# Optimization experiments

Hardware: AMD Instinct MI355X
Metric: run time of the kernel (lower is better)

Reference implementation:

```python
import jax, jax.numpy as jnp
import numpy as np

N = 100000   # nodes
E = 1600000  # edges
G = 64       # graphs in batch
D = 128      # node_dim
H = 128      # hid_dim
OUT = 10     # out_dim (classes)
L = 3        # max_layer GIN layers per branch
BN_EPS = 1e-5


def setup_inputs() -> dict:
    key = jax.random.key(0)
    ks = jax.random.split(key, 24)
    p = lambda k, shape: (jax.random.normal(k, shape, jnp.float32) * 0.05)
    inp = {
        "x": jax.random.normal(ks[0], (N, D), jnp.float32),
        "edge_index": jax.random.randint(ks[1], (2, E), 0, N, jnp.int32),
        "batch": jnp.sort(jax.random.randint(ks[2], (N,), 0, G, jnp.int32)),
        # branch A: conv1 + convs  (stacked per-layer params; node_dim == hid_dim)
        "W1a": p(ks[3], (L, D, H)), "b1a": p(ks[4], (L, H)),
        "W2a": p(ks[5], (L, H, H)), "b2a": p(ks[6], (L, H)),
        "ga": jnp.ones((L, H), jnp.float32), "bta": jnp.zeros((L, H), jnp.float32),
        # branch B: conv2 + convs2
        "W1b": p(ks[7], (L, D, H)), "b1b": p(ks[8], (L, H)),
        "W2b": p(ks[9], (L, H, H)), "b2b": p(ks[10], (L, H)),
        "gb": jnp.ones((L, H), jnp.float32), "btb": jnp.zeros((L, H), jnp.float32),
        # heads
        "lin1_w": p(ks[11], (2 * H, H)), "lin1_b": p(ks[12], (H,)),
        "lin2_w": p(ks[13], (H, OUT)), "lin2_b": p(ks[14], (OUT,)),
        # bilinear discriminator (nn.Bilinear(H, H, 1))
        "disc_w": p(ks[15], (H, H)), "disc_b": jnp.zeros((), jnp.float32),
    }
    return inp


def _gin(h, src, dst, W1, b1, W2, b2, g, bt):
    # GINConv (eps=0): MLP(x + sum_{j->i} x_j); MLP = Lin-ReLU-Lin-ReLU-BN
    agg = jax.ops.segment_sum(h[src], dst, num_segments=N)  # scatter-add over edges
    h = h + agg
    h = jax.nn.relu(h @ W1 + b1)
    h = jax.nn.relu(h @ W2 + b2)
    mu = h.mean(0)
    var = jnp.mean((h - mu) ** 2, axis=0)
    return (h - mu) * jax.lax.rsqrt(var + BN_EPS) * g + bt


def reference(x, edge_index, batch, W1a, b1a, W2a, b2a, ga, bta,
              W1b, b1b, W2b, b2b, gb, btb, lin1_w, lin1_b, lin2_w, lin2_b,
              disc_w, disc_b):
    src, dst = edge_index[0], edge_index[1]
    counts = jnp.clip(jax.ops.segment_sum(jnp.ones((N,), x.dtype), batch, num_segments=G), 1.0)

    # branch A: conv1 + convs -> per-graph mean pool
    h = x
    for i in range(L):
        h = _gin(h, src, dst, W1a[i], b1a[i], W2a[i], b2a[i], ga[i], bta[i])
    mean_a = jax.ops.segment_sum(h, batch, num_segments=G) / counts[:, None]  # [G,H]

    # branch B (subgraph branch, run on the same graph): conv2 + convs2 -> pool
    hb = x
    for i in range(L):
        hb = _gin(hb, src, dst, W1b[i], b1b[i], W2b[i], b2b[i], gb[i], btb[i])
    pool_x = jax.ops.segment_sum(hb, batch, num_segments=G) / counts[:, None]  # [G,H]

    # MI discriminator: shuffle index as in Net.MI
    idx = jnp.arange(G - 1, -1, -1)
    idx = idx.at[G // 2].set(idx[G // 2 + 1])
    shuffled = pool_x[idx]
    bil = lambda a, c: jnp.einsum('gd,de,ge->g', a, disc_w, c) + disc_b
    logits = jnp.concatenate([bil(pool_x, pool_x), bil(pool_x, shuffled)])  # [2G]

    # classification head: cat(mean_pool, pool_x) -> lin1 -> relu -> lin2 -> log_softmax
    z = jnp.concatenate([mean_a, pool_x], axis=-1)
    z = jax.nn.relu(z @ lin1_w + lin1_b)
    z = z @ lin2_w + lin2_b
    predicts = jax.nn.log_softmax(z, axis=-1)  # [G,OUT]

    return jnp.concatenate([predicts.ravel(), logits.ravel()])  # [G*OUT + 2G]
```

## Files before the change

### kernel.cpp

```cpp
#include <hip/hip_runtime.h>
#include <hip/hip_bf16.h>

#define NN 100000
#define EE 1600000
#define GG 64
#define HH 128
#define LL 3
#define BN_EPS 1e-5f
#define NBUCK 196
#define BCAP 12288
#define PART_CHUNK 8192
#define NREP 16

typedef __attribute__((ext_vector_type(8))) short bf16x8;
typedef __attribute__((ext_vector_type(4))) float f32x4;
typedef unsigned int uint32;

__device__ __forceinline__ unsigned short f2bf(float f) {
    uint32 x = __float_as_uint(f);
    uint32 r = (x + 0x7fffu + ((x >> 16) & 1u)) >> 16;
    return (unsigned short)r;
}
__device__ __forceinline__ float bf2f(unsigned short u) { return __uint_as_float(((uint32)u) << 16); }
__device__ __forceinline__ void accq(float4& a, uint32 u, float sc) {
    a.x += sc * (float)(u & 0xffu);
    a.y += sc * (float)((u >> 8) & 0xffu);
    a.z += sc * (float)((u >> 16) & 0xffu);
    a.w += sc * (float)(u >> 24);
}
__device__ __forceinline__ uint32 ld32(const unsigned char* p, uint32 off) {
    return *(const uint32*)(p + off);
}
__device__ __forceinline__ float ldf(const float* p, uint32 byteoff) {
    return *(const float*)((const char*)p + byteoff);
}

__global__ __launch_bounds__(256) void partition_kernel(
    const int* __restrict__ src, const int* __restrict__ dst,
    int* __restrict__ bcnt, uint32* __restrict__ part) {
    __shared__ int cnt[NBUCK];
    __shared__ int loff[NBUCK + 1];
    __shared__ int gpos[NBUCK];
    __shared__ int lcur[NBUCK];
    __shared__ uint32 buf[PART_CHUNK];
    int tid = threadIdx.x;
    int base = blockIdx.x * PART_CHUNK;
    int n = min(PART_CHUNK, EE - base);
    for (int i = tid; i < NBUCK; i += 256) { cnt[i] = 0; lcur[i] = 0; }
    __syncthreads();
    for (int i = tid; i < n; i += 256) atomicAdd(&cnt[dst[base + i] >> 9], 1);
    __syncthreads();
    if (tid == 0) {
        int acc = 0;
        for (int b = 0; b < NBUCK; ++b) { loff[b] = acc; acc += cnt[b]; }
        loff[NBUCK] = acc;
    }
    __syncthreads();
    if (tid < NBUCK && cnt[tid] > 0) gpos[tid] = atomicAdd(&bcnt[tid], cnt[tid]);
    __syncthreads();
    for (int i = tid; i < n; i += 256) {
        int d = dst[base + i];
        int s = src[base + i];
        int b = d >> 9;
        int slot = atomicAdd(&lcur[b], 1);
        buf[loff[b] + slot] = (uint32)s | ((uint32)(d & 511) << 17);
    }
    __syncthreads();
    for (int i = tid; i < n; i += 256) {
        int lo = 0, hi = NBUCK;
        while (hi - lo > 1) { int mid = (lo + hi) >> 1; if (loff[mid] <= i) lo = mid; else hi = mid; }
        part[(size_t)lo * BCAP + gpos[lo] + (i - loff[lo])] = buf[i];
    }
}

__global__ __launch_bounds__(256) void build_col_kernel(
    const uint32* __restrict__ part, const int* __restrict__ bcnt,
    int* __restrict__ col, int2* __restrict__ rowpair) {
    __shared__ int ldeg[512];
    __shared__ int loffn[512];
    __shared__ int lcur[512];
    __shared__ int pscan[256];
    __shared__ int cl[BCAP];
    int b = blockIdx.x;
    int tid = threadIdx.x;
    int node0 = b << 9;
    int nn = min(node0 + 512, NN) - node0;
    int cnt = bcnt[b];
    int base = b * BCAP;
    const uint32* pp = part + (size_t)base;
    for (int i = tid; i < 512; i += 256) { ldeg[i] = 0; lcur[i] = 0; }
    __syncthreads();
    for (int i = tid; i < cnt; i += 256) atomicAdd(&ldeg[pp[i] >> 17], 1);
    __syncthreads();
    int t2 = tid * 2;
    int a0 = ldeg[t2], a1 = ldeg[t2 + 1];
    int ps = a0 + a1;
    pscan[tid] = ps;
    __syncthreads();
    for (int off = 1; off < 256; off <<= 1) {
        int v = (tid >= off) ? pscan[tid - off] : 0;
        __syncthreads();
        pscan[tid] += v;
        __syncthreads();
    }
    int eo = pscan[tid] - ps;
    loffn[t2] = eo;
    loffn[t2 + 1] = eo + a0;
    if (t2 < nn)     rowpair[node0 + t2]     = make_int2(base + eo, base + eo + a0);
    if (t2 + 1 < nn) rowpair[node0 + t2 + 1] = make_int2(base + eo + a0, base + eo + a0 + a1);
    __syncthreads();
    for (int i = tid; i < cnt; i += 256) {
        uint32 v = pp[i];
        int dl = (int)(v >> 17);
        int pos = atomicAdd(&lcur[dl], 1);
        cl[loffn[dl] + pos] = (int)(v & 0x1FFFFu);
    }
    __syncthreads();
    for (int i = tid; i < cnt; i += 256) col[base + i] = cl[i];
}

__global__ void counts_kernel(const int* __restrict__ batch, float* __restrict__ cnt, int n) {
    __shared__ int h[GG];
    int tid = threadIdx.x;
    if (tid < GG) h[tid] = 0;
    __syncthreads();
    int i = blockIdx.x * 256 + tid;
    if (i < n) atomicAdd(&h[batch[i]], 1);
    __syncthreads();
    if (tid < GG && h[tid]) atomicAdd(&cnt[tid], (float)h[tid]);
}

__global__ void x_to_i8_kernel(const float* __restrict__ x, unsigned short* __restrict__ x8,
                               float* __restrict__ sc0) {
    int row = (blockIdx.x * 256 + threadIdx.x) >> 6;
    int lane = threadIdx.x & 63;
    if (row >= NN) return;
    float2 v = ((const float2*)x)[(size_t)row * 64 + lane];
    float m = fmaxf(fabsf(v.x), fabsf(v.y));
#pragma unroll
    for (int off = 1; off < 64; off <<= 1) m = fmaxf(m, __shfl_xor(m, off));
    float scale = m * (1.f / 127.f);
    float inv = (m > 0.f) ? 127.f / m : 0.f;
    int b0 = __float2int_rn(v.x * inv) + 128;
    int b1 = __float2int_rn(v.y * inv) + 128;
    unsigned short pk = (unsigned short)((b0 & 0xff) | ((b1 & 0xff) << 8));
    x8[(size_t)row * 64 + lane] = pk;
    if (lane == 0) sc0[row] = scale;
}

#define MAT_STRIDE 16384

__global__ void convert_w_kernel(const float* __restrict__ W1a, const float* __restrict__ W2a,
                                 const float* __restrict__ W1b, const float* __restrict__ W2b,
                                 unsigned short* __restrict__ out) {
    int t = blockIdx.x * 256 + threadIdx.x;
    if (t >= 24576) return;
    int lane = t & 63;
    int r = t >> 6;
    int ks = r & 3; r >>= 2;
    int nt = r & 7; r >>= 3;
    int mat = r & 1; r >>= 1;
    int l = r % 3, br = r / 3;
    const float* W = br ? (mat ? W2b : W1b) : (mat ? W2a : W1a);
    const float* Wl = W + (size_t)l * 128 * 128;
    int n0 = nt * 16 + (lane & 15);
    int k0 = ks * 32 + (lane >> 4) * 8;
    unsigned short tmp[8];
#pragma unroll
    for (int j = 0; j < 8; ++j) tmp[j] = f2bf(Wl[(size_t)(k0 + j) * 128 + n0]);
    size_t seq = (size_t)(br * 3 + l) * 2 + mat;
    size_t off = (((seq * 8 + nt) * 4 + ks) * 64 + (size_t)lane) * 8;
    *(uint4*)(out + off) = *(const uint4*)tmp;
}

__global__ void bn_coefs_kernel(const float* __restrict__ statsRep,
                                const float* __restrict__ ga, const float* __restrict__ bta,
                                const float* __restrict__ gb, const float* __restrict__ btb,
                                int l, float* __restrict__ coef) {
    int t = threadIdx.x;
    int br = t >> 7, cc = t & 127;
    const float* base = statsRep + (size_t)((l * 2 + br) * NREP) * 256;
    float s = 0.f, sq = 0.f;
#pragma unroll
    for (int rep = 0; rep < NREP; ++rep) {
        s += base[rep * 256 + cc];
        sq += base[rep * 256 + 128 + cc];
    }
    float mu = s * (1.f / NN);
    float var = sq * (1.f / NN) - mu * mu;
    float gm = (br ? gb : ga)[l * 128 + cc];
    float A = gm * rsqrtf(var + BN_EPS);
    float B = (br ? btb : bta)[l * 128 + cc] - mu * A;
    coef[br * 256 + cc] = A;
    coef[br * 256 + 128 + cc] = B;
}

__global__ __launch_bounds__(256) void gather0_kernel(
    const unsigned char* __restrict__ x8b, const float* __restrict__ sc0,
    const int2* __restrict__ rowpair, const int* __restrict__ col,
    uint2* __restrict__ out) {
    int gw = (blockIdx.x * blockDim.x + threadIdx.x) >> 6;
    int lane = threadIdx.x & 63;
    if (gw >= NN) return;
    int slot = lane >> 5;
    int c = lane & 31;
    uint32 c4 = (uint32)c << 2;
    float4 accA = {0.f, 0.f, 0.f, 0.f};
    float4 accB = {0.f, 0.f, 0.f, 0.f};
    float S = 0.f;
    if (slot == 0) {
        float s = sc0[gw];
        uint32 u = ld32(x8b, ((uint32)gw << 7) + c4);
        accq(accA, u, s);
        S += s;
    }
    int2 be = rowpair[gw];
    int beg = be.x, end = be.y;
    for (int base = beg; base < end; base += 64) {
        int nb = min(64, end - base);
        int colv = col[base + min(lane, nb - 1)];
        int k = 0;
        for (; k + 4 <= nb; k += 4) {
            int j0 = __shfl(colv, k + slot);
            int j1 = __shfl(colv, k + 2 + slot);
            float s0 = ldf(sc0, (uint32)j0 << 2);
            float s1 = ldf(sc0, (uint32)j1 << 2);
            uint32 u0 = ld32(x8b, ((uint32)j0 << 7) + c4);
            uint32 u1 = ld32(x8b, ((uint32)j1 << 7) + c4);
            accq(accA, u0, s0); S += s0;
            accq(accB, u1, s1); S += s1;
        }
        for (; k + 2 <= nb; k += 2) {
            int j = __shfl(colv, k + slot);
            float s = ldf(sc0, (uint32)j << 2);
            uint32 u = ld32(x8b, ((uint32)j << 7) + c4);
            accq(accA, u, s); S += s;
        }
        if (k < nb) {
            int j = __shfl(colv, k);
            if (slot == 0) {
                float s = ldf(sc0, (uint32)j << 2);
                uint32 u = ld32(x8b, ((uint32)j << 7) + c4);
                accq(accA, u, s); S += s;
            }
        }
    }
    accA.x += accB.x; accA.y += accB.y; accA.z += accB.z; accA.w += accB.w;
    accA.x += __shfl_xor(accA.x, 32);
    accA.y += __shfl_xor(accA.y, 32);
    accA.z += __shfl_xor(accA.z, 32);
    accA.w += __shfl_xor(accA.w, 32);
    S += __shfl_xor(S, 32);
    float f0 = accA.x - 128.f * S;
    float f1 = accA.y - 128.f * S;
    float f2 = accA.z - 128.f * S;
    float f3 = accA.w - 128.f * S;
    if (slot == 0) {
        uint2 o;
        o.x = (uint32)f2bf(f0) | ((uint32)f2bf(f1) << 16);
        o.y = (uint32)f2bf(f2) | ((uint32)f2bf(f3) << 16);
        out[(uint32)gw * 32 + c] = o;
    }
}

__global__ __launch_bounds__(256) void gather_dual_kernel(
    const unsigned char* __restrict__ y8, const float* __restrict__ scales,
    const int2* __restrict__ rowpair, const int* __restrict__ col,
    const float* __restrict__ coef, uint2* __restrict__ out) {
    int gw = (blockIdx.x * blockDim.x + threadIdx.x) >> 6;
    int lane = threadIdx.x & 63;
    if (gw >= NN) return;
    int br = lane >> 5;
    int c32 = lane & 31;
    uint32 ln4 = (uint32)lane << 2;
    uint32 sb4 = (uint32)br << 2;
    float4 A4 = ((const float4*)(coef + br * 256))[c32];
    float4 B4 = ((const float4*)(coef + br * 256 + 128))[c32];
    float4 accA = {0.f, 0.f, 0.f, 0.f};
    float4 accB = {0.f, 0.f, 0.f, 0.f};
    {
        float s = ldf(scales, ((uint32)gw << 3) + sb4);
        uint32 u = ld32(y8, ((uint32)gw << 8) + ln4);
        accq(accA, u, s);
    }
    int2 be = rowpair[gw];
    int beg = be.x, end = be.y;
    float degp1 = (float)(end - beg + 1);
    for (int base = beg; base < end; base += 64) {
        int nb = min(64, end - base);
        int colv = col[base + min(lane, nb - 1)];
        int k = 0;
        for (; k + 4 <= nb; k += 4) {
            int j0 = __builtin_amdgcn_readlane(colv, k);
            int j1 = __builtin_amdgcn_readlane(colv, k + 1);
            int j2 = __builtin_amdgcn_readlane(colv, k + 2);
            int j3 = __builtin_amdgcn_readlane(colv, k + 3);
            float s0 = ldf(scales, ((uint32)j0 << 3) + sb4);
            float s1 = ldf(scales, ((uint32)j1 << 3) + sb4);
            float s2 = ldf(scales, ((uint32)j2 << 3) + sb4);
            float s3 = ldf(scales, ((uint32)j3 << 3) + sb4);
            uint32 u0 = ld32(y8, ((uint32)j0 << 8) + ln4);
            uint32 u1 = ld32(y8, ((uint32)j1 << 8) + ln4);
            uint32 u2 = ld32(y8, ((uint32)j2 << 8) + ln4);
            uint32 u3 = ld32(y8, ((uint32)j3 << 8) + ln4);
            accq(accA, u0, s0);
            accq(accB, u1, s1);
            accq(accA, u2, s2);
            accq(accB, u3, s3);
        }
        for (; k < nb; ++k) {
            int j = __builtin_amdgcn_readlane(colv, k);
            float s = ldf(scales, ((uint32)j << 3) + sb4);
            uint32 u = ld32(y8, ((uint32)j << 8) + ln4);
            accq(accA, u, s);
        }
    }
    float o0 = A4.x * (accA.x + accB.x) + B4.x * degp1;
    float o1 = A4.y * (accA.y + accB.y) + B4.y * degp1;
    float o2 = A4.z * (accA.z + accB.z) + B4.z * degp1;
    float o3 = A4.w * (accA.w + accB.w) + B4.w * degp1;
    uint2 o;
    o.x = (uint32)f2bf(o0) | ((uint32)f2bf(o1) << 16);
    o.y = (uint32)f2bf(o2) | ((uint32)f2bf(o3) << 16);
    out[(size_t)gw * 64 + lane] = o;
}

#define LDS_W1 16384
#define LDS_HS (8 * 16 * 136)
__global__ __launch_bounds__(512, 4) void mlp_dual_kernel(
    const unsigned short* __restrict__ X, int in_stride, int in_off_mul,
    const unsigned short* __restrict__ wf_all,
    const float* __restrict__ b1a, const float* __restrict__ b1b,
    const float* __restrict__ b2a, const float* __restrict__ b2b,
    int l, int quant,
    unsigned short* __restrict__ Y, unsigned char* __restrict__ Y8,
    float* __restrict__ scales, float* __restrict__ statsRep, int n) {
    extern __shared__ unsigned short lds_all[];
    unsigned short* w1s = lds_all;
    unsigned short (*hs)[16][136] = (unsigned short (*)[16][136])(lds_all + LDS_W1);
    float* ssum = (float*)(lds_all + LDS_W1 + LDS_HS);
    float* ssq = ssum + 128;

    int br = blockIdx.y;
    const unsigned short* Wf = wf_all + (size_t)(br * 3 + l) * 2 * MAT_STRIDE;
    const float* b1 = (br ? b1b : b1a) + l * 128;
    const float* b2 = (br ? b2b : b2a) + l * 128;
    float* statsp = statsRep + (size_t)((l * 2 + br) * NREP + (blockIdx.x & (NREP - 1))) * 256;
    int in_off = in_off_mul * br;

    int tid = threadIdx.x;
    int wv = tid >> 6, lane = tid & 63;
    int quad = lane >> 4, l16 = lane & 15;

    const bf16x8* w2g = (const bf16x8*)(Wf + MAT_STRIDE);

    bf16x8 w2p[2][4];
#pragma unroll
    for (int p = 0; p < 2; ++p)
#pragma unroll
        for (int ks = 0; ks < 4; ++ks) w2p[p][ks] = w2g[(p * 4 + ks) * 64 + lane];

    int row0 = blockIdx.x * 128 + wv * 16;

    bf16x8 aF[4];
    {
        int r = row0 + l16;
        if (r >= n) r = n - 1;
        const unsigned short* xrow = X + (size_t)r * in_stride + in_off;
#pragma unroll
        for (int ks = 0; ks < 4; ++ks) aF[ks] = *(const bf16x8*)(xrow + ks * 32 + quad * 8);
    }

    {
        const uint4* srcp = (const uint4*)Wf;
        uint4* dstp = (uint4*)w1s;
        for (int i = tid; i < 2048; i += 512) dstp[i] = srcp[i];
    }
    if (tid < 128) { ssum[tid] = 0.f; ssq[tid] = 0.f; }
    __syncthreads();

    f32x4 acc1[8];
#pragma unroll
    for (int nt = 0; nt < 8; ++nt) {
        f32x4 c = {0.f, 0.f, 0.f, 0.f};
#pragma unroll
        for (int ks = 0; ks < 4; ++ks) {
            bf16x8 bfrag = *(const bf16x8*)(&w1s[((nt * 4 + ks) * 64 + lane) * 8]);
            c = __builtin_amdgcn_mfma_f32_16x16x32_bf16(aF[ks], bfrag, c, 0, 0, 0);
        }
        acc1[nt] = c;
    }

#pragma unroll
    for (int nt = 0; nt < 8; ++nt) {
        int c0 = nt * 16 + l16;
        float bb = b1[c0];
#pragma unroll
        for (int r = 0; r < 4; ++r) {
            float v = fmaxf(acc1[nt][r] + bb, 0.f);
            hs[wv][quad * 4 + r][c0] = f2bf(v);
        }
    }

    bf16x8 aH[4];
#pragma unroll
    for (int ks = 0; ks < 4; ++ks)
        aH[ks] = *(const bf16x8*)(&hs[wv][l16][ks * 32 + quad * 8]);

    f32x4 acc2_[8];
#pragma unroll
    for (int nt = 0; nt < 8; ++nt) {
        bf16x8 bf0, bf1, bf2, bf3;
        if (nt < 2) { bf0 = w2p[nt][0]; bf1 = w2p[nt][1]; bf2 = w2p[nt][2]; bf3 = w2p[nt][3]; }
        else {
            bf0 = w2g[(nt * 4 + 0) * 64 + lane];
            bf1 = w2g[(nt * 4 + 1) * 64 + lane];
            bf2 = w2g[(nt * 4 + 2) * 64 + lane];
            bf3 = w2g[(nt * 4 + 3) * 64 + lane];
        }
        f32x4 c = {0.f, 0.f, 0.f, 0.f};
        c = __builtin_amdgcn_mfma_f32_16x16x32_bf16(aH[0], bf0, c, 0, 0, 0);
        c = __builtin_amdgcn_mfma_f32_16x16x32_bf16(aH[1], bf1, c, 0, 0, 0);
        c = __builtin_amdgcn_mfma_f32_16x16x32_bf16(aH[2], bf2, c, 0, 0, 0);
        c = __builtin_amdgcn_mfma_f32_16x16x32_bf16(aH[3], bf3, c, 0, 0, 0);
        acc2_[nt] = c;
    }

#pragma unroll
    for (int nt = 0; nt < 8; ++nt) {
        int c0 = nt * 16 + l16;
        float bb = b2[c0];
        float s = 0.f, sq = 0.f;
#pragma unroll
        for (int r = 0; r < 4; ++r) {
            float v = fmaxf(acc2_[nt][r] + bb, 0.f);
            if (row0 + quad * 4 + r >= n) v = 0.f;
            acc2_[nt][r] = v;
            s += v; sq += v * v;
        }
        s += __shfl_xor(s, 16); s += __shfl_xor(s, 32);
        sq += __shfl_xor(sq, 16); sq += __shfl_xor(sq, 32);
        if (quad == 0) { atomicAdd(&ssum[c0], s); atomicAdd(&ssq[c0], sq); }
    }

    unsigned char* hs8 = (unsigned char*)&hs[wv][0][0];
    if (!quant) {
#pragma unroll
        for (int nt = 0; nt < 8; ++nt) {
            int c0 = nt * 16 + l16;
#pragma unroll
            for (int r = 0; r < 4; ++r) hs[wv][quad * 4 + r][c0] = f2bf(acc2_[nt][r]);
        }
        int grow = row0 + l16;
        if (grow < n) {
#pragma unroll
            for (int j = 0; j < 4; ++j) {
                uint4 v = *(const uint4*)(&hs[wv][l16][quad * 32 + j * 8]);
                *(uint4*)(Y + (size_t)grow * 256 + br * 128 + quad * 32 + j * 8) = v;
            }
        }
    } else {
#pragma unroll
        for (int r = 0; r < 4; ++r) {
            float m = acc2_[0][r];
#pragma unroll
            for (int nt = 1; nt < 8; ++nt) m = fmaxf(m, acc2_[nt][r]);
            m = fmaxf(m, __shfl_xor(m, 1));
            m = fmaxf(m, __shfl_xor(m, 2));
            m = fmaxf(m, __shfl_xor(m, 4));
            m = fmaxf(m, __shfl_xor(m, 8));
            float sc = m * (1.f / 255.f);
            float inv = (m > 0.f) ? 255.f / m : 0.f;
            int grow = row0 + quad * 4 + r;
            if (l16 == r && grow < n) scales[grow * 2 + br] = sc;
#pragma unroll
            for (int nt = 0; nt < 8; ++nt) {
                uint32 u = (uint32)__float2int_rn(acc2_[nt][r] * inv);
                hs8[(quad * 4 + r) * 144 + nt * 16 + l16] = (unsigned char)u;
            }
        }
        int grow = row0 + l16;
        if (grow < n) {
            *(uint4*)(Y8 + (size_t)grow * 256 + br * 128 + quad * 32) =
                *(const uint4*)(hs8 + l16 * 144 + quad * 32);
            *(uint4*)(Y8 + (size_t)grow * 256 + br * 128 + quad * 32 + 16) =
                *(const uint4*)(hs8 + l16 * 144 + quad * 32 + 16);
        }
    }
    __syncthreads();
    if (tid < 128) {
        atomicAdd(&statsp[tid], ssum[tid]);
        atomicAdd(&statsp[128 + tid], ssq[tid]);
    }
}

#define POOL_CHUNK 128
__global__ void pool_dual_kernel(const unsigned short* __restrict__ h,
                                 const float* __restrict__ coef2,
                                 const int* __restrict__ batch,
                                 float* __restrict__ poolA, float* __restrict__ poolB, int n) {
    int t = threadIdx.x;
    int br = t >> 7, cc = t & 127;
    float a = coef2[br * 256 + cc];
    float b = coef2[br * 256 + 128 + cc];
    float* pool = br ? poolB : poolA;

    int i0 = blockIdx.x * POOL_CHUNK;
    if (i0 >= n) return;
    int i1 = min(i0 + POOL_CHUNK, n);
    float acc = 0.f;
    int cur = batch[i0];
    for (int i = i0; i < i1; ++i) {
        int g = batch[i];
        if (g != cur) {
            atomicAdd(&pool[cur * 128 + cc], acc);
            acc = 0.f;
            cur = g;
        }
        acc += a * bf2f(h[(size_t)i * 256 + t]) + b;
    }
    atomicAdd(&pool[cur * 128 + cc], acc);
}

__global__ void disc_kernel(const float* __restrict__ poolB, const float* __restrict__ cnt,
                            const float* __restrict__ W, const float* __restrict__ db,
                            float* __restrict__ out) {
    int g = blockIdx.x, e = threadIdx.x;
    __shared__ float rs[128], rh[128];
    float invc = 1.f / fmaxf(cnt[g], 1.f);
    int gs = (g == 32) ? 30 : (63 - g);
    float invcs = 1.f / fmaxf(cnt[gs], 1.f);
    const float* a = poolB + g * 128;
    float t = 0.f;
    for (int d = 0; d < 128; ++d) t += a[d] * W[d * 128 + e];
    t *= invc;
    rs[e] = t * poolB[g * 128 + e] * invc;
    rh[e] = t * poolB[gs * 128 + e] * invcs;
    __syncthreads();
    for (int s = 64; s > 0; s >>= 1) {
        if (e < s) { rs[e] += rs[e + s]; rh[e] += rh[e + s]; }
        __syncthreads();
    }
    if (e == 0) {
        out[GG * 10 + g] = rs[0] + db[0];
        out[GG * 10 + GG + g] = rh[0] + db[0];
    }
}

__global__ void head_kernel(const float* __restrict__ poolA, const float* __restrict__ poolB,
                            const float* __restrict__ cnt,
                            const float* __restrict__ w1, const float* __restrict__ b1,
                            const float* __restrict__ w2, const float* __restrict__ b2,
                            float* __restrict__ out) {
    int g = blockIdx.x, j = threadIdx.x;
    __shared__ float s1[128];
    __shared__ float s2[10];
    __shared__ float lse;
    float invc = 1.f / fmaxf(cnt[g], 1.f);
    const float* ma = poolA + g * 128;
    const float* px = poolB + g * 128;
    float acc = b1[j];
    for (int k = 0; k < 128; ++k) acc += ma[k] * invc * w1[k * 128 + j];
    for (int k = 0; k < 128; ++k) acc += px[k] * invc * w1[(128 + k) * 128 + j];
    s1[j] = fmaxf(acc, 0.f);
    __syncthreads();
    if (j < 10) {
        float a = b2[j];
        for (int k = 0; k < 128; ++k) a += s1[k] * w2[k * 10 + j];
        s2[j] = a;
    }
    __syncthreads();
    if (j == 0) {
        float m = s2[0];
        for (int o = 1; o < 10; ++o) m = fmaxf(m, s2[o]);
        float se = 0.f;
        for (int o = 0; o < 10; ++o) se += expf(s2[o] - m);
        lse = m + logf(se);
    }
    __syncthreads();
    if (j < 10) out[g * 10 + j] = s2[j] - lse;
}

extern "C" void kernel_launch(void* const* d_in, const int* in_sizes, int n_in,
                              void* d_out, int out_size, void* d_ws, size_t ws_size,
                              hipStream_t stream) {
    const float* x     = (const float*)d_in[0];
    const int*   ei    = (const int*)d_in[1];
    const int*   batch = (const int*)d_in[2];
    const float* W1a = (const float*)d_in[3];
    const float* b1a = (const float*)d_in[4];
    const float* W2a = (const float*)d_in[5];
    const float* b2a = (const float*)d_in[6];
    const float* ga  = (const float*)d_in[7];
    const float* bta = (const float*)d_in[8];
    const float* W1b = (const float*)d_in[9];
    const float* b1b = (const float*)d_in[10];
    const float* W2b = (const float*)d_in[11];
    const float* b2b = (const float*)d_in[12];
    const float* gb  = (const float*)d_in[13];
    const float* btb = (const float*)d_in[14];
    const float* lin1_w = (const float*)d_in[15];
    const float* lin1_b = (const float*)d_in[16];
    const float* lin2_w = (const float*)d_in[17];
    const float* lin2_b = (const float*)d_in[18];
    const float* disc_w = (const float*)d_in[19];
    const float* disc_b = (const float*)d_in[20];
    float* out = (float*)d_out;

    const int* src = ei;
    const int* dst = ei + EE;

    size_t o = 0;
    auto take = [&](size_t b) { size_t p = o; o = (o + b + 255) & ~(size_t)255; return p; };
    uint8_t* w = (uint8_t*)d_ws;
    size_t o_x8   = take((size_t)NN * 128);
    size_t o_sc0  = take((size_t)NN * 4);
    size_t o_g0   = take((size_t)NN * 128 * 2);
    size_t o_bufP = take((size_t)NN * 256 * 2);
    size_t o_gbuf = take((size_t)NN * 256 * 2);
    size_t o_y8a  = take((size_t)NN * 256);
    size_t o_y8b  = take((size_t)NN * 256);
    size_t o_scA  = take((size_t)NN * 2 * 4);
    size_t o_scB  = take((size_t)NN * 2 * 4);
    size_t o_wf   = take((size_t)12 * MAT_STRIDE * 2);
    size_t o_col  = take((size_t)NBUCK * BCAP * 4);
    size_t o_part = take((size_t)NBUCK * BCAP * 4);
    size_t o_rowpair = take((size_t)NN * 8);
    size_t o_coef = take((size_t)3 * 2 * 256 * 4);
    size_t zero_begin = o;
    size_t o_bcnt   = take((size_t)NBUCK * 4);
    size_t o_stats  = take((size_t)6 * NREP * 256 * 4);
    size_t o_cnt    = take(GG * 4);
    size_t o_poolA  = take((size_t)GG * 128 * 4);
    size_t o_poolB  = take((size_t)GG * 128 * 4);
    size_t zero_end = o;

    unsigned short* x8 = (unsigned short*)(w + o_x8);
    float* sc0 = (float*)(w + o_sc0);
    uint32* g0 = (uint32*)(w + o_g0);
    unsigned short* bufP = (unsigned short*)(w + o_bufP);
    unsigned short* gbuf = (unsigned short*)(w + o_gbuf);
    unsigned char* y8a = (unsigned char*)(w + o_y8a);
    unsigned char* y8b = (unsigned char*)(w + o_y8b);
    float* scA = (float*)(w + o_scA);
    float* scB = (float*)(w + o_scB);
    unsigned short* wf = (unsigned short*)(w + o_wf);
    int* col = (int*)(w + o_col);
    uint32* part = (uint32*)(w + o_part);
    int2* rowpair = (int2*)(w + o_rowpair);
    float* coef = (float*)(w + o_coef);
    int* bcnt = (int*)(w + o_bcnt);
    float* statsRep = (float*)(w + o_stats);
    float* cnt = (float*)(w + o_cnt);
    float* poolA = (float*)(w + o_poolA);
    float* poolB = (float*)(w + o_poolB);

    hipMemsetAsync(w + zero_begin, 0, zero_end - zero_begin, stream);

    x_to_i8_kernel<<<(NN * 64 + 255) / 256, 256, 0, stream>>>(x, x8, sc0);
    convert_w_kernel<<<(24576 + 255) / 256, 256, 0, stream>>>(W1a, W2a, W1b, W2b, wf);

    partition_kernel<<<(EE + PART_CHUNK - 1) / PART_CHUNK, 256, 0, stream>>>(src, dst, bcnt, part);
    build_col_kernel<<<NBUCK, 256, 0, stream>>>(part, bcnt, col, rowpair);
    counts_kernel<<<(NN + 255) / 256, 256, 0, stream>>>(batch, cnt, NN);

    int gatherBlocks = (NN + 3) / 4;
    dim3 mlpGrid((NN + 127) / 128, 2);
    size_t ldsBytes = (size_t)LDS_W1 * 2 + (size_t)LDS_HS * 2 + 256 * 4;

    gather0_kernel<<<gatherBlocks, 256, 0, stream>>>(
        (const unsigned char*)x8, sc0, rowpair, col, (uint2*)g0);

    mlp_dual_kernel<<<mlpGrid, 512, ldsBytes, stream>>>(
        (const unsigned short*)g0, 128, 0, wf, b1a, b1b, b2a, b2b, 0, 1,
        nullptr, y8a, scA, statsRep, NN);
    bn_coefs_kernel<<<1, 256, 0, stream>>>(statsRep, ga, bta, gb, btb, 0, coef + 0 * 512);

    gather_dual_kernel<<<gatherBlocks, 256, 0, stream>>>(
        y8a, scA, rowpair, col, coef + 0 * 512, (uint2*)gbuf);
    mlp_dual_kernel<<<mlpGrid, 512, ldsBytes, stream>>>(
        gbuf, 256, 128, wf, b1a, b1b, b2a, b2b, 1, 1,
        nullptr, y8b, scB, statsRep, NN);
    bn_coefs_kernel<<<1, 256, 0, stream>>>(statsRep, ga, bta, gb, btb, 1, coef + 1 * 512);

    gather_dual_kernel<<<gatherBlocks, 256, 0, stream>>>(
        y8b, scB, rowpair, col, coef + 1 * 512, (uint2*)gbuf);
    mlp_dual_kernel<<<mlpGrid, 512, ldsBytes, stream>>>(
        gbuf, 256, 128, wf, b1a, b1b, b2a, b2b, 2, 0,
        bufP, nullptr, nullptr, statsRep, NN);
    bn_coefs_kernel<<<1, 256, 0, stream>>>(statsRep, ga, bta, gb, btb, 2, coef + 2 * 512);

    pool_dual_kernel<<<(NN + POOL_CHUNK - 1) / POOL_CHUNK, 256, 0, stream>>>(
        bufP, coef + 2 * 512, batch, poolA, poolB, NN);
    disc_kernel<<<GG, 128, 0, stream>>>(poolB, cnt, disc_w, disc_b, out);
    head_kernel<<<GG, 128, 0, stream>>>(poolA, poolB, cnt, lin1_w, lin1_b, lin2_w, lin2_b, out);
}
```

Before: 658.0 us.

## Fuse mean-pool into last MLP layer and apply BN affine after pooling

The final MLP layer no longer writes the bf16 node buffer. It accumulates raw per-graph sums into LDS and then into a global per-graph array with atomics. The BatchNorm affine is applied to the pooled sums in the head and discriminator kernels (A*sum + B*count), and the separate pool kernel is removed. W1 is now read straight from global memory instead of being staged in LDS, which raises the launch-bounds occupancy target. The LDS pool assumes each 128-node block spans at most four graphs (clamped), which holds for sorted batch ids with large graphs.

```diff
diff --git a/kernel.cpp b/kernel.cpp
--- a/kernel.cpp
+++ b/kernel.cpp
@@ -325,24 +325,26 @@
     out[(size_t)gw * 64 + lane] = o;
 }
 
-#define LDS_W1 16384
 #define LDS_HS (8 * 16 * 136)
-__global__ __launch_bounds__(512, 4) void mlp_dual_kernel(
+#define GSPAN 4
+__global__ __launch_bounds__(512, 8) void mlp_dual_kernel(
     const unsigned short* __restrict__ X, int in_stride, int in_off_mul,
     const unsigned short* __restrict__ wf_all,
     const float* __restrict__ b1a, const float* __restrict__ b1b,
     const float* __restrict__ b2a, const float* __restrict__ b2b,
     int l, int quant,
-    unsigned short* __restrict__ Y, unsigned char* __restrict__ Y8,
+    const int* __restrict__ batch, float* __restrict__ Sg,
+    unsigned char* __restrict__ Y8,
     float* __restrict__ scales, float* __restrict__ statsRep, int n) {
     extern __shared__ unsigned short lds_all[];
-    unsigned short* w1s = lds_all;
-    unsigned short (*hs)[16][136] = (unsigned short (*)[16][136])(lds_all + LDS_W1);
-    float* ssum = (float*)(lds_all + LDS_W1 + LDS_HS);
+    unsigned short (*hs)[16][136] = (unsigned short (*)[16][136])lds_all;
+    float* ssum = (float*)(lds_all + LDS_HS);
     float* ssq = ssum + 128;
 
     int br = blockIdx.y;
     const unsigned short* Wf = wf_all + (size_t)(br * 3 + l) * 2 * MAT_STRIDE;
+    const bf16x8* w1g = (const bf16x8*)Wf;
+    const bf16x8* w2g = (const bf16x8*)(Wf + MAT_STRIDE);
     const float* b1 = (br ? b1b : b1a) + l * 128;
     const float* b2 = (br ? b2b : b2a) + l * 128;
     float* statsp = statsRep + (size_t)((l * 2 + br) * NREP + (blockIdx.x & (NREP - 1))) * 256;
@@ -351,14 +353,6 @@
     int tid = threadIdx.x;
     int wv = tid >> 6, lane = tid & 63;
     int quad = lane >> 4, l16 = lane & 15;
-
-    const bf16x8* w2g = (const bf16x8*)(Wf + MAT_STRIDE);
-
-    bf16x8 w2p[2][4];
-#pragma unroll
-    for (int p = 0; p < 2; ++p)
-#pragma unroll
-        for (int ks = 0; ks < 4; ++ks) w2p[p][ks] = w2g[(p * 4 + ks) * 64 + lane];
 
     int row0 = blockIdx.x * 128 + wv * 16;
 
@@ -371,11 +365,6 @@
         for (int ks = 0; ks < 4; ++ks) aF[ks] = *(const bf16x8*)(xrow + ks * 32 + quad * 8);
     }
 
-    {
-        const uint4* srcp = (const uint4*)Wf;
-        uint4* dstp = (uint4*)w1s;
-        for (int i = tid; i < 2048; i += 512) dstp[i] = srcp[i];
-    }
     if (tid < 128) { ssum[tid] = 0.f; ssq[tid] = 0.f; }
     __syncthreads();
 
@@ -384,10 +373,8 @@
     for (int nt = 0; nt < 8; ++nt) {
         f32x4 c = {0.f, 0.f, 0.f, 0.f};
 #pragma unroll
-        for (int ks = 0; ks < 4; ++ks) {
-            bf16x8 bfrag = *(const bf16x8*)(&w1s[((nt * 4 + ks) * 64 + lane) * 8]);
-            c = __builtin_amdgcn_mfma_f32_16x16x32_bf16(aF[ks], bfrag, c, 0, 0, 0);
-        }
+        for (int ks = 0; ks < 4; ++ks)
+            c = __builtin_amdgcn_mfma_f32_16x16x32_bf16(aF[ks], w1g[(nt * 4 + ks) * 64 + lane], c, 0, 0, 0);
         acc1[nt] = c;
     }
 
@@ -410,19 +397,11 @@
     f32x4 acc2_[8];
 #pragma unroll
     for (int nt = 0; nt < 8; ++nt) {
-        bf16x8 bf0, bf1, bf2, bf3;
-        if (nt < 2) { bf0 = w2p[nt][0]; bf1 = w2p[nt][1]; bf2 = w2p[nt][2]; bf3 = w2p[nt][3]; }
-        else {
-            bf0 = w2g[(nt * 4 + 0) * 64 + lane];
-            bf1 = w2g[(nt * 4 + 1) * 64 + lane];
-            bf2 = w2g[(nt * 4 + 2) * 64 + lane];
-            bf3 = w2g[(nt * 4 + 3) * 64 + lane];
-        }
         f32x4 c = {0.f, 0.f, 0.f, 0.f};
-        c = __builtin_amdgcn_mfma_f32_16x16x32_bf16(aH[0], bf0, c, 0, 0, 0);
-        c = __builtin_amdgcn_mfma_f32_16x16x32_bf16(aH[1], bf1, c, 0, 0, 0);
-        c = __builtin_amdgcn_mfma_f32_16x16x32_bf16(aH[2], bf2, c, 0, 0, 0);
-        c = __builtin_amdgcn_mfma_f32_16x16x32_bf16(aH[3], bf3, c, 0, 0, 0);
+        c = __builtin_amdgcn_mfma_f32_16x16x32_bf16(aH[0], w2g[(nt * 4 + 0) * 64 + lane], c, 0, 0, 0);
+        c = __builtin_amdgcn_mfma_f32_16x16x32_bf16(aH[1], w2g[(nt * 4 + 1) * 64 + lane], c, 0, 0, 0);
+        c = __builtin_amdgcn_mfma_f32_16x16x32_bf16(aH[2], w2g[(nt * 4 + 2) * 64 + lane], c, 0, 0, 0);
+        c = __builtin_amdgcn_mfma_f32_16x16x32_bf16(aH[3], w2g[(nt * 4 + 3) * 64 + lane], c, 0, 0, 0);
         acc2_[nt] = c;
     }
 
@@ -443,23 +422,8 @@
         if (quad == 0) { atomicAdd(&ssum[c0], s); atomicAdd(&ssq[c0], sq); }
     }
 
-    unsigned char* hs8 = (unsigned char*)&hs[wv][0][0];
-    if (!quant) {
-#pragma unroll
-        for (int nt = 0; nt < 8; ++nt) {
-            int c0 = nt * 16 + l16;
-#pragma unroll
-            for (int r = 0; r < 4; ++r) hs[wv][quad * 4 + r][c0] = f2bf(acc2_[nt][r]);
-        }
-        int grow = row0 + l16;
-        if (grow < n) {
-#pragma unroll
-            for (int j = 0; j < 4; ++j) {
-                uint4 v = *(const uint4*)(&hs[wv][l16][quad * 32 + j * 8]);
-                *(uint4*)(Y + (size_t)grow * 256 + br * 128 + quad * 32 + j * 8) = v;
-            }
-        }
-    } else {
+    if (quant) {
+        unsigned char* hs8 = (unsigned char*)&hs[wv][0][0];
 #pragma unroll
         for (int r = 0; r < 4; ++r) {
             float m = acc2_[0][r];
@@ -486,6 +450,38 @@
             *(uint4*)(Y8 + (size_t)grow * 256 + br * 128 + quad * 32 + 16) =
                 *(const uint4*)(hs8 + l16 * 144 + quad * 32 + 16);
         }
+    } else {
+        __syncthreads();
+        float* pl = (float*)lds_all;
+        for (int i = tid; i < GSPAN * 128; i += 512) pl[i] = 0.f;
+        __syncthreads();
+        int gmin = batch[blockIdx.x * 128];
+        int gidx[4];
+#pragma unroll
+        for (int r = 0; r < 4; ++r) {
+            int node = row0 + quad * 4 + r;
+            int gi = -1;
+            if (node < n) {
+                gi = batch[node] - gmin;
+                if (gi < 0) gi = 0;
+                if (gi > GSPAN - 1) gi = GSPAN - 1;
+            }
+            gidx[r] = gi;
+        }
+#pragma unroll
+        for (int nt = 0; nt < 8; ++nt) {
+            int c0 = nt * 16 + l16;
+#pragma unroll
+            for (int r = 0; r < 4; ++r)
+                if (gidx[r] >= 0) atomicAdd(&pl[gidx[r] * 128 + c0], acc2_[nt][r]);
+        }
+        __syncthreads();
+        for (int i = tid; i < GSPAN * 128; i += 512) {
+            float v = pl[i];
+            int g = gmin + (i >> 7);
+            if (v != 0.f && g < GG)
+                atomicAdd(&Sg[(size_t)br * GG * 128 + g * 128 + (i & 127)], v);
+        }
     }
     __syncthreads();
     if (tid < 128) {
@@ -494,48 +490,25 @@
     }
 }
 
-#define POOL_CHUNK 128
-__global__ void pool_dual_kernel(const unsigned short* __restrict__ h,
-                                 const float* __restrict__ coef2,
-                                 const int* __restrict__ batch,
-                                 float* __restrict__ poolA, float* __restrict__ poolB, int n) {
-    int t = threadIdx.x;
-    int br = t >> 7, cc = t & 127;
-    float a = coef2[br * 256 + cc];
-    float b = coef2[br * 256 + 128 + cc];
-    float* pool = br ? poolB : poolA;
-
-    int i0 = blockIdx.x * POOL_CHUNK;
-    if (i0 >= n) return;
-    int i1 = min(i0 + POOL_CHUNK, n);
-    float acc = 0.f;
-    int cur = batch[i0];
-    for (int i = i0; i < i1; ++i) {
-        int g = batch[i];
-        if (g != cur) {
-            atomicAdd(&pool[cur * 128 + cc], acc);
-            acc = 0.f;
-            cur = g;
-        }
-        acc += a * bf2f(h[(size_t)i * 256 + t]) + b;
-    }
-    atomicAdd(&pool[cur * 128 + cc], acc);
-}
-
-__global__ void disc_kernel(const float* __restrict__ poolB, const float* __restrict__ cnt,
+__global__ void disc_kernel(const float* __restrict__ Sg, const float* __restrict__ cnt,
+                            const float* __restrict__ coefL2,
                             const float* __restrict__ W, const float* __restrict__ db,
                             float* __restrict__ out) {
     int g = blockIdx.x, e = threadIdx.x;
-    __shared__ float rs[128], rh[128];
+    __shared__ float pg[128], ps[128], rs[128], rh[128];
     float invc = 1.f / fmaxf(cnt[g], 1.f);
     int gs = (g == 32) ? 30 : (63 - g);
     float invcs = 1.f / fmaxf(cnt[gs], 1.f);
-    const float* a = poolB + g * 128;
+    float Ab = coefL2[256 + e], Bb = coefL2[384 + e];
+    const float* SB = Sg + (size_t)GG * 128;
+    pg[e] = Ab * SB[g * 128 + e] + Bb * cnt[g];
+    ps[e] = Ab * SB[gs * 128 + e] + Bb * cnt[gs];
+    __syncthreads();
     float t = 0.f;
-    for (int d = 0; d < 128; ++d) t += a[d] * W[d * 128 + e];
+    for (int d = 0; d < 128; ++d) t += pg[d] * W[d * 128 + e];
     t *= invc;
-    rs[e] = t * poolB[g * 128 + e] * invc;
-    rh[e] = t * poolB[gs * 128 + e] * invcs;
+    rs[e] = t * pg[e] * invc;
+    rh[e] = t * ps[e] * invcs;
     __syncthreads();
     for (int s = 64; s > 0; s >>= 1) {
         if (e < s) { rs[e] += rs[e + s]; rh[e] += rh[e + s]; }
@@ -547,21 +520,26 @@
     }
 }
 
-__global__ void head_kernel(const float* __restrict__ poolA, const float* __restrict__ poolB,
-                            const float* __restrict__ cnt,
+__global__ void head_kernel(const float* __restrict__ Sg, const float* __restrict__ cnt,
+                            const float* __restrict__ coefL2,
                             const float* __restrict__ w1, const float* __restrict__ b1,
                             const float* __restrict__ w2, const float* __restrict__ b2,
                             float* __restrict__ out) {
     int g = blockIdx.x, j = threadIdx.x;
+    __shared__ float ma[128], px[128];
     __shared__ float s1[128];
     __shared__ float s2[10];
     __shared__ float lse;
-    float invc = 1.f / fmaxf(cnt[g], 1.f);
-    const float* ma = poolA + g * 128;
-    const float* px = poolB + g * 128;
+    float cg = cnt[g];
+    float invc = 1.f / fmaxf(cg, 1.f);
+    float Aa = coefL2[j],       Ba = coefL2[128 + j];
+    float Ab = coefL2[256 + j], Bb = coefL2[384 + j];
+    ma[j] = (Aa * Sg[g * 128 + j] + Ba * cg) * invc;
+    px[j] = (Ab * Sg[(size_t)GG * 128 + g * 128 + j] + Bb * cg) * invc;
+    __syncthreads();
     float acc = b1[j];
-    for (int k = 0; k < 128; ++k) acc += ma[k] * invc * w1[k * 128 + j];
-    for (int k = 0; k < 128; ++k) acc += px[k] * invc * w1[(128 + k) * 128 + j];
+    for (int k = 0; k < 128; ++k) acc += ma[k] * w1[k * 128 + j];
+    for (int k = 0; k < 128; ++k) acc += px[k] * w1[(128 + k) * 128 + j];
     s1[j] = fmaxf(acc, 0.f);
     __syncthreads();
     if (j < 10) {
@@ -616,7 +594,6 @@
     size_t o_x8   = take((size_t)NN * 128);
     size_t o_sc0  = take((size_t)NN * 4);
     size_t o_g0   = take((size_t)NN * 128 * 2);
-    size_t o_bufP = take((size_t)NN * 256 * 2);
     size_t o_gbuf = take((size_t)NN * 256 * 2);
     size_t o_y8a  = take((size_t)NN * 256);
     size_t o_y8b  = take((size_t)NN * 256);
@@ -631,14 +608,12 @@
     size_t o_bcnt   = take((size_t)NBUCK * 4);
     size_t o_stats  = take((size_t)6 * NREP * 256 * 4);
     size_t o_cnt    = take(GG * 4);
-    size_t o_poolA  = take((size_t)GG * 128 * 4);
-    size_t o_poolB  = take((size_t)GG * 128 * 4);
+    size_t o_Sg     = take((size_t)2 * GG * 128 * 4);
     size_t zero_end = o;
 
     unsigned short* x8 = (unsigned short*)(w + o_x8);
     float* sc0 = (float*)(w + o_sc0);
     uint32* g0 = (uint32*)(w + o_g0);
-    unsigned short* bufP = (unsigned short*)(w + o_bufP);
     unsigned short* gbuf = (unsigned short*)(w + o_gbuf);
     unsigned char* y8a = (unsigned char*)(w + o_y8a);
     unsigned char* y8b = (unsigned char*)(w + o_y8b);
@@ -652,8 +627,7 @@
     int* bcnt = (int*)(w + o_bcnt);
     float* statsRep = (float*)(w + o_stats);
     float* cnt = (float*)(w + o_cnt);
-    float* poolA = (float*)(w + o_poolA);
-    float* poolB = (float*)(w + o_poolB);
+    float* Sg = (float*)(w + o_Sg);
 
     hipMemsetAsync(w + zero_begin, 0, zero_end - zero_begin, stream);
 
@@ -666,32 +640,30 @@
 
     int gatherBlocks = (NN + 3) / 4;
     dim3 mlpGrid((NN + 127) / 128, 2);
-    size_t ldsBytes = (size_t)LDS_W1 * 2 + (size_t)LDS_HS * 2 + 256 * 4;
+    size_t ldsBytes = (size_t)LDS_HS * 2 + 256 * 4;
 
     gather0_kernel<<<gatherBlocks, 256, 0, stream>>>(
         (const unsigned char*)x8, sc0, rowpair, col, (uint2*)g0);
 
     mlp_dual_kernel<<<mlpGrid, 512, ldsBytes, stream>>>(
         (const unsigned short*)g0, 128, 0, wf, b1a, b1b, b2a, b2b, 0, 1,
-        nullptr, y8a, scA, statsRep, NN);
+        batch, Sg, y8a, scA, statsRep, NN);
     bn_coefs_kernel<<<1, 256, 0, stream>>>(statsRep, ga, bta, gb, btb, 0, coef + 0 * 512);
 
     gather_dual_kernel<<<gatherBlocks, 256, 0, stream>>>(
         y8a, scA, rowpair, col, coef + 0 * 512, (uint2*)gbuf);
     mlp_dual_kernel<<<mlpGrid, 512, ldsBytes, stream>>>(
         gbuf, 256, 128, wf, b1a, b1b, b2a, b2b, 1, 1,
-        nullptr, y8b, scB, statsRep, NN);
+        batch, Sg, y8b, scB, statsRep, NN);
     bn_coefs_kernel<<<1, 256, 0, stream>>>(statsRep, ga, bta, gb, btb, 1, coef + 1 * 512);
 
     gather_dual_kernel<<<gatherBlocks, 256, 0, stream>>>(
         y8b, scB, rowpair, col, coef + 1 * 512, (uint2*)gbuf);
     mlp_dual_kernel<<<mlpGrid, 512, ldsBytes, stream>>>(
         gbuf, 256, 128, wf, b1a, b1b, b2a, b2b, 2, 0,
-        bufP, nullptr, nullptr, statsRep, NN);
+        batch, Sg, nullptr, nullptr, statsRep, NN);
     bn_coefs_kernel<<<1, 256, 0, stream>>>(statsRep, ga, bta, gb, btb, 2, coef + 2 * 512);
 
-    pool_dual_kernel<<<(NN + POOL_CHUNK - 1) / POOL_CHUNK, 256, 0, stream>>>(
-        bufP, coef + 2 * 512, batch, poolA, poolB, NN);
-    disc_kernel<<<GG, 128, 0, stream>>>(poolB, cnt, disc_w, disc_b, out);
-    head_kernel<<<GG, 128, 0, stream>>>(poolA, poolB, cnt, lin1_w, lin1_b, lin2_w, lin2_b, out);
-}
+    disc_kernel<<<GG, 128, 0, stream>>>(Sg, cnt, coef + 2 * 512, disc_w, disc_b, out);
+    head_kernel<<<GG, 128, 0, stream>>>(Sg, cnt, coef + 2 * 512, lin1_w, lin1_b, lin2_w, lin2_b, out);
+}
```

Result: slower. 754.2 us (+14.6%).
